# Performance work log

Hardware: AMD Instinct MI355X
Metric: run time of the kernel (lower is better)

The kernel has to match this reference:

```python
import jax, jax.numpy as jnp
import numpy as np

B, T, D = 4, 2048, 1024
H, DK = 8, 64
EPS = 1e-6

def _xavier(key, shape):
    fan_in, fan_out = shape[1], shape[0]
    lim = float(np.sqrt(6.0 / (fan_in + fan_out)))
    return jax.random.uniform(key, shape, jnp.float32, -lim, lim)

def setup_inputs() -> dict:
    key = jax.random.key(0)
    ks = jax.random.split(key, 7)
    x = jax.random.normal(ks[0], (B, T, D), jnp.float32)
    W_Q = _xavier(ks[1], (H * DK, D))
    W_K = _xavier(ks[2], (H * DK, D))
    W_V = _xavier(ks[3], (H * DK, D))
    W_g_w = _xavier(ks[4], (H * DK, D))
    W_g_b = jax.random.normal(ks[5], (H * DK,), jnp.float32) * 0.02
    W_O = _xavier(ks[6], (D, H * DK))
    decay_log = jnp.zeros((H,), jnp.float32)
    return {"x": x, "W_Q": W_Q, "W_K": W_K, "W_V": W_V,
            "W_g_w": W_g_w, "W_g_b": W_g_b, "W_O": W_O,
            "decay_log": decay_log}

def _phi(u):
    # ELU + 1 feature map (positive)
    return jax.nn.elu(u) + 1.0

def reference(x, W_Q, W_K, W_V, W_g_w, W_g_b, W_O, decay_log):
    b, t, d = x.shape
    q = _phi((x @ W_Q.T).reshape(b, t, H, DK))
    k = _phi((x @ W_K.T).reshape(b, t, H, DK))
    v = (x @ W_V.T).reshape(b, t, H, DK)
    gamma = jax.nn.sigmoid(decay_log)           # [H]
    g4 = gamma[None, :, None, None]             # [1,H,1,1]
    g3 = gamma[None, :, None]                   # [1,H,1]

    # time-major for scan: [T,B,H,DK]
    qT = jnp.moveaxis(q, 1, 0)
    kT = jnp.moveaxis(k, 1, 0)
    vT = jnp.moveaxis(v, 1, 0)

    S0 = jnp.zeros((b, H, DK, DK), x.dtype)
    z0 = jnp.zeros((b, H, DK), x.dtype)

    def step(carry, inp):
        S, z = carry
        qt, kt, vt = inp
        S = g4 * S + jnp.einsum('bhi,bhj->bhij', kt, vt)
        z = g3 * z + kt
        num = jnp.einsum('bhij,bhi->bhj', S, qt)
        den = jnp.sum(z * qt, axis=-1, keepdims=True) + EPS
        return (S, z), num / den

    _, ys = jax.lax.scan(step, (S0, z0), (qT, kT, vT))  # ys: [T,B,H,DK]
    outputs = jnp.moveaxis(ys, 0, 1)                    # [B,T,H,DK]

    gate = jax.nn.sigmoid(x @ W_g_w.T + W_g_b).reshape(b, t, H, DK)
    y = (outputs * gate).reshape(b, t, H * DK)
    return y @ W_O.T
```

## Files before the change

kernel.cpp:

```cpp
#include <hip/hip_runtime.h>
#include <cstdint>
#include <cstddef>

#define B_   4
#define T_   2048
#define D_   1024
#define H_   8
#define DK_  64
#define HD_  512
#define CH_  64
#define NC_  32
#define EPS_ 1e-6f

typedef __attribute__((ext_vector_type(4))) float f32x4;
typedef __attribute__((ext_vector_type(8))) short s16x8;

__device__ __forceinline__ unsigned short f2bf(float f) {
    unsigned int x = __float_as_uint(f);
    unsigned int r = (x + 0x7FFFu + ((x >> 16) & 1u)) >> 16;
    return (unsigned short)r;
}
__device__ __forceinline__ float bf2f(unsigned short u) {
    return __uint_as_float(((unsigned int)u) << 16);
}
__device__ __forceinline__ void ld4(const float* p, float* o) {
    float4 v = *(const float4*)p; o[0]=v.x; o[1]=v.y; o[2]=v.z; o[3]=v.w;
}
__device__ __forceinline__ void gl_lds16(const unsigned short* g, unsigned short* l) {
    __builtin_amdgcn_global_load_lds(
        (const __attribute__((address_space(1))) unsigned int*)g,
        (__attribute__((address_space(3))) unsigned int*)l, 16, 0, 0);
}

__global__ __launch_bounds__(256) void k_cvt_all(
    const float* __restrict__ x,
    const float* __restrict__ wq, const float* __restrict__ wk,
    const float* __restrict__ wv, const float* __restrict__ wgw,
    const float* __restrict__ wo,
    unsigned short* __restrict__ xb,
    unsigned short* __restrict__ wqb, unsigned short* __restrict__ wkb,
    unsigned short* __restrict__ wvb, unsigned short* __restrict__ wgb,
    unsigned short* __restrict__ wob)
{
    int bid = blockIdx.x;
    const float* src; unsigned short* dst; int idx;
    if (bid < 8192) {
        src = x; dst = xb; idx = bid * 256 + threadIdx.x;
    } else {
        int r = bid - 8192;
        int w = r >> 9;
        idx = (r & 511) * 256 + threadIdx.x;
        switch (w) {
            case 0:  src = wq;  dst = wqb; break;
            case 1:  src = wk;  dst = wkb; break;
            case 2:  src = wv;  dst = wvb; break;
            case 3:  src = wgw; dst = wgb; break;
            default: src = wo;  dst = wob; break;
        }
    }
    float4 v = ((const float4*)src)[idx];
    ushort4 o;
    o.x = f2bf(v.x); o.y = f2bf(v.y); o.z = f2bf(v.z); o.w = f2bf(v.w);
    ((ushort4*)dst)[idx] = o;
}

__global__ __launch_bounds__(512, 2) void k_gemm_qkvg(
    const unsigned short* __restrict__ xb,
    const unsigned short* __restrict__ wqb, const unsigned short* __restrict__ wkb,
    const unsigned short* __restrict__ wvb, const unsigned short* __restrict__ wgb,
    const float* __restrict__ bias,
    unsigned short* __restrict__ qo, unsigned short* __restrict__ ko,
    unsigned short* __restrict__ vo, unsigned short* __restrict__ go)
{
    __shared__ unsigned short As[2][256 * 64];
    __shared__ unsigned short Bs[2][256 * 64];
    const int tid = threadIdx.x;
    const int id  = blockIdx.x;
    const int xcd = id & 7, per = id >> 3;
    const int mtile = xcd * 4 + (per & 3);
    const int ntile = per >> 2;
    const int which = ntile >> 1;
    const int nb    = ntile & 1;
    const int m0    = mtile * 256;
    const int n0    = nb * 256;
    const unsigned short* Wp = (which == 0) ? wqb : (which == 1) ? wkb : (which == 2) ? wvb : wgb;
    unsigned short* Op       = (which == 0) ? qo  : (which == 1) ? ko  : (which == 2) ? vo  : go;
    const int K = D_;
    const int NIT = K / 64;

    const int lane = tid & 63, wave = tid >> 6;
    const int wm = (wave >> 2) * 128, wn = (wave & 3) * 64;
    const int r16 = lane & 15, quad = lane >> 4;
    const int lrow = lane >> 3, lseg = lane & 7;
    const int sseg = lseg ^ lrow;
    const int rx   = r16 & 7;

    f32x4 acc[8][4];
    #pragma unroll
    for (int a = 0; a < 8; a++)
        #pragma unroll
        for (int b = 0; b < 4; b++) acc[a][b] = 0.0f;

    auto stage = [&](int buf, int ko_) {
        #pragma unroll
        for (int i = 0; i < 4; i++) {
            int chunk = wave * 4 + i;
            int row = chunk * 8 + lrow;
            gl_lds16(xb + (size_t)(m0 + row) * K + ko_ + sseg * 8, &As[buf][chunk * 512]);
            gl_lds16(Wp + (size_t)(n0 + row) * K + ko_ + sseg * 8, &Bs[buf][chunk * 512]);
        }
    };

    stage(0, 0);
    for (int it = 0; it < NIT; ++it) {
        if (it + 1 < NIT) {
            stage((it + 1) & 1, (it + 1) * 64);
            asm volatile("s_waitcnt vmcnt(8)" ::: "memory");
        } else {
            asm volatile("s_waitcnt vmcnt(0)" ::: "memory");
        }
        __builtin_amdgcn_s_barrier();
        const int buf = it & 1;
        #pragma unroll
        for (int kk = 0; kk < 64; kk += 32) {
            const int gb_ = kk >> 3;
            s16x8 af[8], bf[4];
            #pragma unroll
            for (int mt = 0; mt < 8; mt++)
                af[mt] = *(const s16x8*)&As[buf][(wm + mt * 16 + r16) * 64 + (((gb_ + quad) ^ rx) << 3)];
            #pragma unroll
            for (int nt = 0; nt < 4; nt++)
                bf[nt] = *(const s16x8*)&Bs[buf][(wn + nt * 16 + r16) * 64 + (((gb_ + quad) ^ rx) << 3)];
            #pragma unroll
            for (int mt = 0; mt < 8; mt++)
                #pragma unroll
                for (int nt = 0; nt < 4; nt++)
                    acc[mt][nt] = __builtin_amdgcn_mfma_f32_16x16x32_bf16(af[mt], bf[nt], acc[mt][nt], 0, 0, 0);
        }
        __builtin_amdgcn_s_barrier();
    }
    #pragma unroll
    for (int mt = 0; mt < 8; mt++) {
        #pragma unroll
        for (int nt = 0; nt < 4; nt++) {
            int col = n0 + wn + nt * 16 + r16;
            float bv = (which == 3) ? bias[col] : 0.0f;
            #pragma unroll
            for (int r = 0; r < 4; r++) {
                int row = m0 + wm + mt * 16 + quad * 4 + r;
                float v = acc[mt][nt][r];
                if (which <= 1)      v = (v > 0.0f) ? v + 1.0f : __builtin_expf(v);
                else if (which == 3) v = 1.0f / (1.0f + __builtin_expf(-(v + bv)));
                Op[(size_t)row * HD_ + col] = f2bf(v);
            }
        }
    }
}

__global__ __launch_bounds__(512, 2) void k_gemm_out(
    const unsigned short* __restrict__ ogb, const unsigned short* __restrict__ wob,
    float* __restrict__ y)
{
    __shared__ unsigned short As[2][256 * 64];
    __shared__ unsigned short Bs[2][128 * 64];
    const int tid = threadIdx.x;
    const int id  = blockIdx.x;
    const int xcd = id & 7, per = id >> 3;
    const int m0 = (xcd * 4 + (per & 3)) * 256;
    const int n0 = (per >> 2) * 128;
    const int K = HD_;
    const int NIT = K / 64;

    const int lane = tid & 63, wave = tid >> 6;
    const int wm = (wave >> 1) * 64, wn = (wave & 1) * 64;
    const int r16 = lane & 15, quad = lane >> 4;
    const int lrow = lane >> 3, lseg = lane & 7;
    const int sseg = lseg ^ lrow;
    const int rx   = r16 & 7;

    f32x4 acc[4][4];
    #pragma unroll
    for (int a = 0; a < 4; a++)
        #pragma unroll
        for (int b = 0; b < 4; b++) acc[a][b] = 0.0f;

    auto stage = [&](int buf, int ko_) {
        #pragma unroll
        for (int i = 0; i < 4; i++) {
            int chunk = wave * 4 + i;
            int row = chunk * 8 + lrow;
            gl_lds16(ogb + (size_t)(m0 + row) * K + ko_ + sseg * 8, &As[buf][chunk * 512]);
        }
        #pragma unroll
        for (int i = 0; i < 2; i++) {
            int chunk = wave * 2 + i;
            int row = chunk * 8 + lrow;
            gl_lds16(wob + (size_t)(n0 + row) * K + ko_ + sseg * 8, &Bs[buf][chunk * 512]);
        }
    };

    stage(0, 0);
    for (int it = 0; it < NIT; ++it) {
        if (it + 1 < NIT) {
            stage((it + 1) & 1, (it + 1) * 64);
            asm volatile("s_waitcnt vmcnt(6)" ::: "memory");
        } else {
            asm volatile("s_waitcnt vmcnt(0)" ::: "memory");
        }
        __builtin_amdgcn_s_barrier();
        const int buf = it & 1;
        #pragma unroll
        for (int kk = 0; kk < 64; kk += 32) {
            const int gb_ = kk >> 3;
            s16x8 af[4], bf[4];
            #pragma unroll
            for (int mt = 0; mt < 4; mt++)
                af[mt] = *(const s16x8*)&As[buf][(wm + mt * 16 + r16) * 64 + (((gb_ + quad) ^ rx) << 3)];
            #pragma unroll
            for (int nt = 0; nt < 4; nt++)
                bf[nt] = *(const s16x8*)&Bs[buf][(wn + nt * 16 + r16) * 64 + (((gb_ + quad) ^ rx) << 3)];
            #pragma unroll
            for (int mt = 0; mt < 4; mt++)
                #pragma unroll
                for (int nt = 0; nt < 4; nt++)
                    acc[mt][nt] = __builtin_amdgcn_mfma_f32_16x16x32_bf16(af[mt], bf[nt], acc[mt][nt], 0, 0, 0);
        }
        __builtin_amdgcn_s_barrier();
    }
    #pragma unroll
    for (int mt = 0; mt < 4; mt++)
        #pragma unroll
        for (int nt = 0; nt < 4; nt++) {
            int col = n0 + wn + nt * 16 + r16;
            #pragma unroll
            for (int r = 0; r < 4; r++) {
                int row = m0 + wm + mt * 16 + quad * 4 + r;
                y[(size_t)row * D_ + col] = acc[mt][nt][r];
            }
        }
}

__global__ __launch_bounds__(256) void k_chunk_sums(
    const unsigned short* __restrict__ Kb, const unsigned short* __restrict__ Vb,
    float* __restrict__ Ssum, float* __restrict__ zsum, const float* __restrict__ decay_log)
{
    __shared__ float kl[CH_ * 68];
    __shared__ float vl[CH_ * 68];
    const int tid = threadIdx.x;
    const int bc  = blockIdx.x;
    const int c   = bc & (NC_ - 1);
    const int bh  = bc >> 5;
    const int h   = bh & (H_ - 1);
    const int b   = bh >> 3;
    const float g  = 1.0f / (1.0f + __builtin_expf(-decay_log[h]));
    const float lg = __builtin_log2f(g);
    const int t0 = c * CH_;

    #pragma unroll
    for (int e = 0; e < 2; e++) {
        int lid = e * 256 + tid;
        int l = lid >> 3, d0 = (lid & 7) * 8;
        float w = __builtin_exp2f((float)(CH_ - 1 - l) * lg);
        size_t gidx = (size_t)(b * T_ + t0 + l) * HD_ + h * DK_ + d0;
        uint4 kraw = *(const uint4*)(Kb + gidx);
        uint4 vraw = *(const uint4*)(Vb + gidx);
        const unsigned short* kp = (const unsigned short*)&kraw;
        const unsigned short* vp = (const unsigned short*)&vraw;
        #pragma unroll
        for (int j = 0; j < 8; j++) {
            kl[l * 68 + d0 + j] = bf2f(kp[j]) * w;
            vl[l * 68 + d0 + j] = bf2f(vp[j]);
        }
    }
    __syncthreads();

    const int ti = tid & 15, tj = tid >> 4;
    const int i0 = ti * 4, j0 = tj * 4;
    float acc[4][4];
    #pragma unroll
    for (int r = 0; r < 4; r++)
        #pragma unroll
        for (int cc = 0; cc < 4; cc++) acc[r][cc] = 0.0f;

    for (int l = 0; l < CH_; l++) {
        float kv[4], vv[4];
        ld4(&kl[l * 68 + i0], kv);
        ld4(&vl[l * 68 + j0], vv);
        #pragma unroll
        for (int r = 0; r < 4; r++)
            #pragma unroll
            for (int cc = 0; cc < 4; cc++) acc[r][cc] += kv[r] * vv[cc];
    }
    size_t base = (size_t)bc * (DK_ * DK_);
    #pragma unroll
    for (int cc = 0; cc < 4; cc++) {
        float4 st = make_float4(acc[0][cc], acc[1][cc], acc[2][cc], acc[3][cc]);
        *(float4*)&Ssum[base + (size_t)(j0 + cc) * DK_ + i0] = st;
    }
    if (tid < DK_) {
        float s = 0.0f;
        for (int l = 0; l < CH_; l++) s += kl[l * 68 + tid];
        zsum[(size_t)bc * DK_ + tid] = s;
    }
}

__global__ __launch_bounds__(128) void k_chunk_scan(
    float* __restrict__ Ssum, float* __restrict__ zsum, const float* __restrict__ decay_log)
{
    const int tid = threadIdx.x;
    const int grp = blockIdx.x & 31;
    const int bh  = blockIdx.x >> 5;
    const int h   = bh & (H_ - 1);
    const float g  = 1.0f / (1.0f + __builtin_expf(-decay_log[h]));
    const float gC = __builtin_exp2f((float)CH_ * __builtin_log2f(g));
    int elem = grp * 128 + tid;
    float s = 0.0f;
    for (int c = 0; c < NC_; c++) {
        size_t idx = ((size_t)(bh * NC_ + c)) * 4096 + elem;
        float v = Ssum[idx];
        Ssum[idx] = s;
        s = gC * s + v;
    }
    if (grp == 0 && tid < DK_) {
        float z = 0.0f;
        for (int c = 0; c < NC_; c++) {
            size_t idx = ((size_t)(bh * NC_ + c)) * DK_ + tid;
            float v = zsum[idx];
            zsum[idx] = z;
            z = gC * z + v;
        }
    }
}

__global__ __launch_bounds__(256) void k_chunk_out(
    const unsigned short* __restrict__ Qb, const unsigned short* __restrict__ Kb,
    const unsigned short* __restrict__ Vb, const unsigned short* __restrict__ Gb,
    const float* __restrict__ Ssum, const float* __restrict__ zsum,
    unsigned short* __restrict__ OGb, const float* __restrict__ decay_log)
{
    __shared__ unsigned short ql[64 * 72];
    __shared__ unsigned short kl[64 * 72];
    __shared__ unsigned short sT[64 * 72];
    __shared__ float scT[64 * 68];
    __shared__ float vf [64 * 68];
    __shared__ float ogl[64 * 68];
    __shared__ float den_l[64];
    __shared__ float zp[64];
    __shared__ float gpow[CH_ + 1];

    const int tid = threadIdx.x;
    const int bc  = blockIdx.x;
    const int c   = bc & (NC_ - 1);
    const int bh  = bc >> 5;
    const int h   = bh & (H_ - 1);
    const int b   = bh >> 3;
    const float g  = 1.0f / (1.0f + __builtin_expf(-decay_log[h]));
    const float lg = __builtin_log2f(g);
    const int t0 = c * CH_;

    if (tid <= CH_) gpow[tid] = __builtin_exp2f((float)tid * lg);
    if (tid < DK_)  zp[tid] = zsum[(size_t)bc * DK_ + tid];

    #pragma unroll
    for (int e = 0; e < 2; e++) {
        int lid = e * 256 + tid;
        int l = lid >> 3, d0 = (lid & 7) * 8;
        size_t gidx = (size_t)(b * T_ + t0 + l) * HD_ + h * DK_ + d0;
        uint4 qraw = *(const uint4*)(Qb + gidx);
        uint4 kraw = *(const uint4*)(Kb + gidx);
        uint4 vraw = *(const uint4*)(Vb + gidx);
        *(uint4*)&ql[l * 72 + d0] = qraw;
        *(uint4*)&kl[l * 72 + d0] = kraw;
        const unsigned short* vp = (const unsigned short*)&vraw;
        #pragma unroll
        for (int j = 0; j < 8; j++) vf[l * 68 + d0 + j] = bf2f(vp[j]);
    }
    {
        int j = tid >> 2, seg = tid & 3;
        const float4* src = (const float4*)&Ssum[(size_t)bc * 4096 + (size_t)j * 64 + seg * 16];
        #pragma unroll
        for (int e = 0; e < 4; e++) {
            float4 a4 = src[e];
            ushort4 o;
            o.x = f2bf(a4.x); o.y = f2bf(a4.y); o.z = f2bf(a4.z); o.w = f2bf(a4.w);
            *(ushort4*)&sT[j * 72 + seg * 16 + e * 4] = o;
        }
    }
    __syncthreads();

    const int lane = tid & 63, wave = tid >> 6;
    const int r16 = lane & 15, quad = lane >> 4;
    const int ibase = 16 * wave;

    f32x4 sc4[4];
    #pragma unroll
    for (int lt = 0; lt < 4; lt++) {
        f32x4 s = 0.0f;
        #pragma unroll
        for (int ks = 0; ks < 2; ks++) {
            s16x8 af  = *(const s16x8*)&ql[(ibase + r16) * 72 + ks * 32 + quad * 8];
            s16x8 bf_ = *(const s16x8*)&kl[(16 * lt + r16) * 72 + ks * 32 + quad * 8];
            s = __builtin_amdgcn_mfma_f32_16x16x32_bf16(af, bf_, s, 0, 0, 0);
        }
        sc4[lt] = s;
    }
    float rs[4] = {0.0f, 0.0f, 0.0f, 0.0f};
    #pragma unroll
    for (int lt = 0; lt < 4; lt++) {
        int l = 16 * lt + r16;
        #pragma unroll
        for (int rr = 0; rr < 4; rr++) {
            int i = ibase + quad * 4 + rr;
            float val = (l <= i) ? sc4[lt][rr] * gpow[i - l] : 0.0f;
            scT[l * 68 + i] = val;
            rs[rr] += val;
        }
    }
    #pragma unroll
    for (int rr = 0; rr < 4; rr++) {
        float v_ = rs[rr];
        v_ += __shfl_xor(v_, 1);
        v_ += __shfl_xor(v_, 2);
        v_ += __shfl_xor(v_, 4);
        v_ += __shfl_xor(v_, 8);
        if (r16 == 0) den_l[ibase + quad * 4 + rr] = v_;
    }
    #pragma unroll
    for (int jt = 0; jt < 4; jt++) {
        f32x4 o = 0.0f;
        #pragma unroll
        for (int ks = 0; ks < 2; ks++) {
            s16x8 af  = *(const s16x8*)&ql[(ibase + r16) * 72 + ks * 32 + quad * 8];
            s16x8 bf_ = *(const s16x8*)&sT[(16 * jt + r16) * 72 + ks * 32 + quad * 8];
            o = __builtin_amdgcn_mfma_f32_16x16x32_bf16(af, bf_, o, 0, 0, 0);
        }
        #pragma unroll
        for (int rr = 0; rr < 4; rr++) {
            int i = ibase + quad * 4 + rr;
            ogl[i * 68 + 16 * jt + r16] = o[rr] * gpow[i + 1];
        }
    }
    __syncthreads();

    if (tid < DK_) {
        float dp = 0.0f;
        #pragma unroll
        for (int d8 = 0; d8 < 8; d8++) {
            uint4 qq = *(const uint4*)&ql[tid * 72 + d8 * 8];
            const unsigned short* qp = (const unsigned short*)&qq;
            #pragma unroll
            for (int e = 0; e < 8; e++) dp += bf2f(qp[e]) * zp[d8 * 8 + e];
        }
        den_l[tid] += gpow[tid + 1] * dp + EPS_;
    }
    __syncthreads();

    const int ti = tid >> 4, tj = tid & 15;
    const int i0 = ti * 4, j0 = tj * 4;
    float og[4][4];
    #pragma unroll
    for (int r = 0; r < 4; r++) ld4(&ogl[(i0 + r) * 68 + j0], og[r]);

    for (int l = 0; l < CH_; l++) {
        float scv[4], vv[4];
        ld4(&scT[l * 68 + i0], scv);
        ld4(&vf[l * 68 + j0], vv);
        #pragma unroll
        for (int r = 0; r < 4; r++)
            #pragma unroll
            for (int cc = 0; cc < 4; cc++) og[r][cc] += scv[r] * vv[cc];
    }
    #pragma unroll
    for (int r = 0; r < 4; r++) {
        int i = i0 + r;
        float rcp = 1.0f / den_l[i];
        size_t gidx = (size_t)(b * T_ + t0 + i) * HD_ + h * DK_ + j0;
        ushort4 graw = *(const ushort4*)(Gb + gidx);
        ushort4 o;
        o.x = f2bf(og[r][0] * rcp * bf2f(graw.x));
        o.y = f2bf(og[r][1] * rcp * bf2f(graw.y));
        o.z = f2bf(og[r][2] * rcp * bf2f(graw.z));
        o.w = f2bf(og[r][3] * rcp * bf2f(graw.w));
        *(ushort4*)(OGb + gidx) = o;
    }
}

extern "C" void kernel_launch(void* const* d_in, const int* in_sizes, int n_in,
                              void* d_out, int out_size, void* d_ws, size_t ws_size,
                              hipStream_t stream)
{
    (void)in_sizes; (void)n_in; (void)out_size; (void)ws_size;
    const float* x         = (const float*)d_in[0];
    const float* W_Q       = (const float*)d_in[1];
    const float* W_K       = (const float*)d_in[2];
    const float* W_V       = (const float*)d_in[3];
    const float* W_gw      = (const float*)d_in[4];
    const float* W_gb      = (const float*)d_in[5];
    const float* W_O       = (const float*)d_in[6];
    const float* decay_log = (const float*)d_in[7];
    float* y = (float*)d_out;

    char* ws = (char*)d_ws;
    size_t off = 0;
    auto alloc = [&](size_t bytes) { void* p = ws + off; off += (bytes + 255) & ~(size_t)255; return p; };
    unsigned short* xb   = (unsigned short*)alloc((size_t)B_ * T_ * D_ * 2);
    unsigned short* wqb  = (unsigned short*)alloc((size_t)HD_ * D_ * 2);
    unsigned short* wkb  = (unsigned short*)alloc((size_t)HD_ * D_ * 2);
    unsigned short* wvb  = (unsigned short*)alloc((size_t)HD_ * D_ * 2);
    unsigned short* wgb  = (unsigned short*)alloc((size_t)HD_ * D_ * 2);
    unsigned short* wob  = (unsigned short*)alloc((size_t)D_ * HD_ * 2);
    unsigned short* qb   = (unsigned short*)alloc((size_t)B_ * T_ * HD_ * 2);
    unsigned short* kb   = (unsigned short*)alloc((size_t)B_ * T_ * HD_ * 2);
    unsigned short* vb   = (unsigned short*)alloc((size_t)B_ * T_ * HD_ * 2);
    unsigned short* gb   = (unsigned short*)alloc((size_t)B_ * T_ * HD_ * 2);
    unsigned short* ogb  = (unsigned short*)alloc((size_t)B_ * T_ * HD_ * 2);
    float* Ssum = (float*)alloc((size_t)B_ * H_ * NC_ * DK_ * DK_ * 4);
    float* zsum = (float*)alloc((size_t)B_ * H_ * NC_ * DK_ * 4);

    k_cvt_all<<<8192 + 5 * 512, 256, 0, stream>>>(x, W_Q, W_K, W_V, W_gw, W_O,
                                                  xb, wqb, wkb, wvb, wgb, wob);
    k_gemm_qkvg<<<256, 512, 0, stream>>>(xb, wqb, wkb, wvb, wgb, W_gb, qb, kb, vb, gb);
    k_chunk_sums<<<B_ * H_ * NC_, 256, 0, stream>>>(kb, vb, Ssum, zsum, decay_log);
    k_chunk_scan<<<B_ * H_ * NC_, 128, 0, stream>>>(Ssum, zsum, decay_log);
    k_chunk_out<<<B_ * H_ * NC_, 256, 0, stream>>>(qb, kb, vb, gb, Ssum, zsum, ogb, decay_log);
    k_gemm_out<<<256, 512, 0, stream>>>(ogb, wob, y);
}
```

Before: 205.4 us.

## Move chunk-sum and intra-chunk PV products from scalar FMA to bf16 MFMA

The chunk-summary kernel now stores decayed K and V transposed in LDS as bf16 and computes the per-chunk K^T V state with 16x16x32 bf16 MFMA instead of a scalar fp32 outer-product loop. The chunk-output kernel stores the masked, decayed score matrix as bf16 and does the P·V product with MFMA, keeping the inter-chunk result in registers rather than spilling it to an LDS buffer. It also hoists the Q fragment loads so they are reused. This cuts scalar FLOPs and LDS use, but adds bf16 rounding of scores and decayed keys, and the final gated store becomes scalar 2-byte accesses.

```diff
diff --git a/kernel.cpp b/kernel.cpp
--- a/kernel.cpp
+++ b/kernel.cpp
@@ -22,9 +22,6 @@
 }
 __device__ __forceinline__ float bf2f(unsigned short u) {
     return __uint_as_float(((unsigned int)u) << 16);
-}
-__device__ __forceinline__ void ld4(const float* p, float* o) {
-    float4 v = *(const float4*)p; o[0]=v.x; o[1]=v.y; o[2]=v.z; o[3]=v.w;
 }
 __device__ __forceinline__ void gl_lds16(const unsigned short* g, unsigned short* l) {
     __builtin_amdgcn_global_load_lds(
@@ -244,8 +241,8 @@
     const unsigned short* __restrict__ Kb, const unsigned short* __restrict__ Vb,
     float* __restrict__ Ssum, float* __restrict__ zsum, const float* __restrict__ decay_log)
 {
-    __shared__ float kl[CH_ * 68];
-    __shared__ float vl[CH_ * 68];
+    __shared__ unsigned short kt[64 * 72];
+    __shared__ unsigned short vt[64 * 72];
     const int tid = threadIdx.x;
     const int bc  = blockIdx.x;
     const int c   = bc & (NC_ - 1);
@@ -268,38 +265,38 @@
         const unsigned short* vp = (const unsigned short*)&vraw;
         #pragma unroll
         for (int j = 0; j < 8; j++) {
-            kl[l * 68 + d0 + j] = bf2f(kp[j]) * w;
-            vl[l * 68 + d0 + j] = bf2f(vp[j]);
+            kt[(d0 + j) * 72 + l] = f2bf(bf2f(kp[j]) * w);
+            vt[(d0 + j) * 72 + l] = vp[j];
         }
     }
     __syncthreads();
 
-    const int ti = tid & 15, tj = tid >> 4;
-    const int i0 = ti * 4, j0 = tj * 4;
-    float acc[4][4];
-    #pragma unroll
-    for (int r = 0; r < 4; r++)
-        #pragma unroll
-        for (int cc = 0; cc < 4; cc++) acc[r][cc] = 0.0f;
-
-    for (int l = 0; l < CH_; l++) {
-        float kv[4], vv[4];
-        ld4(&kl[l * 68 + i0], kv);
-        ld4(&vl[l * 68 + j0], vv);
-        #pragma unroll
-        for (int r = 0; r < 4; r++)
-            #pragma unroll
-            for (int cc = 0; cc < 4; cc++) acc[r][cc] += kv[r] * vv[cc];
-    }
+    const int lane = tid & 63, wave = tid >> 6;
+    const int r16 = lane & 15, quad = lane >> 4;
     size_t base = (size_t)bc * (DK_ * DK_);
-    #pragma unroll
-    for (int cc = 0; cc < 4; cc++) {
-        float4 st = make_float4(acc[0][cc], acc[1][cc], acc[2][cc], acc[3][cc]);
-        *(float4*)&Ssum[base + (size_t)(j0 + cc) * DK_ + i0] = st;
+
+    #pragma unroll
+    for (int it = 0; it < 4; it++) {
+        f32x4 sacc = 0.0f;
+        #pragma unroll
+        for (int ks = 0; ks < 2; ks++) {
+            s16x8 af  = *(const s16x8*)&vt[(16 * wave + r16) * 72 + ks * 32 + quad * 8];
+            s16x8 bf_ = *(const s16x8*)&kt[(16 * it   + r16) * 72 + ks * 32 + quad * 8];
+            sacc = __builtin_amdgcn_mfma_f32_16x16x32_bf16(af, bf_, sacc, 0, 0, 0);
+        }
+        #pragma unroll
+        for (int rr = 0; rr < 4; rr++)
+            Ssum[base + (size_t)(16 * wave + quad * 4 + rr) * DK_ + 16 * it + r16] = sacc[rr];
     }
     if (tid < DK_) {
         float s = 0.0f;
-        for (int l = 0; l < CH_; l++) s += kl[l * 68 + tid];
+        #pragma unroll
+        for (int l8 = 0; l8 < 8; l8++) {
+            uint4 kk = *(const uint4*)&kt[tid * 72 + l8 * 8];
+            const unsigned short* kp = (const unsigned short*)&kk;
+            #pragma unroll
+            for (int e = 0; e < 8; e++) s += bf2f(kp[e]);
+        }
         zsum[(size_t)bc * DK_ + tid] = s;
     }
 }
@@ -341,9 +338,8 @@
     __shared__ unsigned short ql[64 * 72];
     __shared__ unsigned short kl[64 * 72];
     __shared__ unsigned short sT[64 * 72];
-    __shared__ float scT[64 * 68];
-    __shared__ float vf [64 * 68];
-    __shared__ float ogl[64 * 68];
+    __shared__ unsigned short vt[64 * 72];
+    __shared__ unsigned short pl[64 * 72];
     __shared__ float den_l[64];
     __shared__ float zp[64];
     __shared__ float gpow[CH_ + 1];
@@ -373,7 +369,7 @@
         *(uint4*)&kl[l * 72 + d0] = kraw;
         const unsigned short* vp = (const unsigned short*)&vraw;
         #pragma unroll
-        for (int j = 0; j < 8; j++) vf[l * 68 + d0 + j] = bf2f(vp[j]);
+        for (int j = 0; j < 8; j++) vt[(d0 + j) * 72 + l] = vp[j];
     }
     {
         int j = tid >> 2, seg = tid & 3;
@@ -392,15 +388,19 @@
     const int r16 = lane & 15, quad = lane >> 4;
     const int ibase = 16 * wave;
 
+    s16x8 aq[2];
+    #pragma unroll
+    for (int ks = 0; ks < 2; ks++)
+        aq[ks] = *(const s16x8*)&ql[(ibase + r16) * 72 + ks * 32 + quad * 8];
+
     f32x4 sc4[4];
     #pragma unroll
     for (int lt = 0; lt < 4; lt++) {
         f32x4 s = 0.0f;
         #pragma unroll
         for (int ks = 0; ks < 2; ks++) {
-            s16x8 af  = *(const s16x8*)&ql[(ibase + r16) * 72 + ks * 32 + quad * 8];
             s16x8 bf_ = *(const s16x8*)&kl[(16 * lt + r16) * 72 + ks * 32 + quad * 8];
-            s = __builtin_amdgcn_mfma_f32_16x16x32_bf16(af, bf_, s, 0, 0, 0);
+            s = __builtin_amdgcn_mfma_f32_16x16x32_bf16(aq[ks], bf_, s, 0, 0, 0);
         }
         sc4[lt] = s;
     }
@@ -412,8 +412,9 @@
         for (int rr = 0; rr < 4; rr++) {
             int i = ibase + quad * 4 + rr;
             float val = (l <= i) ? sc4[lt][rr] * gpow[i - l] : 0.0f;
-            scT[l * 68 + i] = val;
-            rs[rr] += val;
+            unsigned short pb = f2bf(val);
+            pl[i * 72 + l] = pb;
+            rs[rr] += bf2f(pb);
         }
     }
     #pragma unroll
@@ -425,23 +426,31 @@
         v_ += __shfl_xor(v_, 8);
         if (r16 == 0) den_l[ibase + quad * 4 + rr] = v_;
     }
+    f32x4 og[4];
     #pragma unroll
     for (int jt = 0; jt < 4; jt++) {
         f32x4 o = 0.0f;
         #pragma unroll
         for (int ks = 0; ks < 2; ks++) {
-            s16x8 af  = *(const s16x8*)&ql[(ibase + r16) * 72 + ks * 32 + quad * 8];
             s16x8 bf_ = *(const s16x8*)&sT[(16 * jt + r16) * 72 + ks * 32 + quad * 8];
-            o = __builtin_amdgcn_mfma_f32_16x16x32_bf16(af, bf_, o, 0, 0, 0);
-        }
-        #pragma unroll
-        for (int rr = 0; rr < 4; rr++) {
-            int i = ibase + quad * 4 + rr;
-            ogl[i * 68 + 16 * jt + r16] = o[rr] * gpow[i + 1];
-        }
+            o = __builtin_amdgcn_mfma_f32_16x16x32_bf16(aq[ks], bf_, o, 0, 0, 0);
+        }
+        #pragma unroll
+        for (int rr = 0; rr < 4; rr++)
+            o[rr] *= gpow[ibase + quad * 4 + rr + 1];
+        og[jt] = o;
     }
     __syncthreads();
 
+    #pragma unroll
+    for (int jt = 0; jt < 4; jt++) {
+        #pragma unroll
+        for (int ks = 0; ks < 2; ks++) {
+            s16x8 ap  = *(const s16x8*)&pl[(ibase + r16) * 72 + ks * 32 + quad * 8];
+            s16x8 bf_ = *(const s16x8*)&vt[(16 * jt + r16) * 72 + ks * 32 + quad * 8];
+            og[jt] = __builtin_amdgcn_mfma_f32_16x16x32_bf16(ap, bf_, og[jt], 0, 0, 0);
+        }
+    }
     if (tid < DK_) {
         float dp = 0.0f;
         #pragma unroll
@@ -455,33 +464,17 @@
     }
     __syncthreads();
 
-    const int ti = tid >> 4, tj = tid & 15;
-    const int i0 = ti * 4, j0 = tj * 4;
-    float og[4][4];
-    #pragma unroll
-    for (int r = 0; r < 4; r++) ld4(&ogl[(i0 + r) * 68 + j0], og[r]);
-
-    for (int l = 0; l < CH_; l++) {
-        float scv[4], vv[4];
-        ld4(&scT[l * 68 + i0], scv);
-        ld4(&vf[l * 68 + j0], vv);
-        #pragma unroll
-        for (int r = 0; r < 4; r++)
-            #pragma unroll
-            for (int cc = 0; cc < 4; cc++) og[r][cc] += scv[r] * vv[cc];
-    }
-    #pragma unroll
-    for (int r = 0; r < 4; r++) {
-        int i = i0 + r;
-        float rcp = 1.0f / den_l[i];
-        size_t gidx = (size_t)(b * T_ + t0 + i) * HD_ + h * DK_ + j0;
-        ushort4 graw = *(const ushort4*)(Gb + gidx);
-        ushort4 o;
-        o.x = f2bf(og[r][0] * rcp * bf2f(graw.x));
-        o.y = f2bf(og[r][1] * rcp * bf2f(graw.y));
-        o.z = f2bf(og[r][2] * rcp * bf2f(graw.z));
-        o.w = f2bf(og[r][3] * rcp * bf2f(graw.w));
-        *(ushort4*)(OGb + gidx) = o;
+    #pragma unroll
+    for (int jt = 0; jt < 4; jt++) {
+        int j = 16 * jt + r16;
+        #pragma unroll
+        for (int rr = 0; rr < 4; rr++) {
+            int i = ibase + quad * 4 + rr;
+            float rcp = 1.0f / den_l[i];
+            size_t ga = (size_t)(b * T_ + t0 + i) * HD_ + h * DK_ + j;
+            float gate = bf2f(Gb[ga]);
+            OGb[ga] = f2bf(og[jt][rr] * rcp * gate);
+        }
     }
 }
 
```

Measured after the change: 197.9 us. 1.04x faster.
